# Kernel optimization log

Measured on AMD Instinct MI355X. Metric: run time of the kernel, lower is better.

The kernel has to match this reference:

```python
import jax, jax.numpy as jnp
import numpy as np

VD, VP, VM = 1958, 1430, 131
E = 64
B, S, ND, NM = 512, 16, 40, 30
SOS = VM  # voc_size[2]


def setup_inputs() -> dict:
    key = jax.random.key(0)
    ks = jax.random.split(key, 16)
    inp = {
        "diseases": jax.random.randint(ks[0], (B, S, ND), 0, VD),
        "procedures": jax.random.randint(ks[1], (B, S, 10), 0, VP),
        "medications": jax.random.randint(ks[2], (B, S, NM), 0, VM),
        "d_mask_matrix": jnp.zeros((B, S, ND), jnp.float32),
        "m_mask_matrix": jnp.zeros((B, S, NM), jnp.float32),
        "seq_length": jax.random.randint(ks[3], (B,), 1, S + 1),
    }
    s = 0.1
    inp["diag_table"] = s * jax.random.normal(ks[4], (VD + 3, E), jnp.float32)
    inp["med_table"] = s * jax.random.normal(ks[5], (VM + 3, E), jnp.float32)
    inp["attn_w"] = s * jax.random.normal(ks[6], (1, 2 * E), jnp.float32)
    inp["attn_b"] = jnp.zeros((1,), jnp.float32)
    inp["gru_w_ih"] = s * jax.random.normal(ks[7], (3 * E, 2 * E), jnp.float32)
    inp["gru_w_hh"] = s * jax.random.normal(ks[8], (3 * E, E), jnp.float32)
    inp["gru_b_ih"] = jnp.zeros((3 * E,), jnp.float32)
    inp["gru_b_hh"] = jnp.zeros((3 * E,), jnp.float32)
    inp["wo_w"] = s * jax.random.normal(ks[9], (VM + 2, E), jnp.float32)
    inp["wo_b"] = jnp.zeros((VM + 2,), jnp.float32)
    return inp


def reference(diseases, procedures, medications, d_mask_matrix, m_mask_matrix,
              seq_length, diag_table, med_table, attn_w, attn_b,
              gru_w_ih, gru_w_hh, gru_b_ih, gru_b_hh, wo_w, wo_b):
    # Training-mode (teacher-forcing) forward; dropout treated as identity (eval of dropout).
    b, s, nm = medications.shape
    e = diag_table.shape[1]
    disease_emb = diag_table[diseases]  # [B,S,Nd,E]
    # teacher-forcing inputs: SOS followed by gold medications
    last_med = jnp.concatenate(
        [jnp.full((b, s, 1), SOS, medications.dtype), medications], axis=2)  # [B,S,Nm+1]
    dec_embs = med_table[last_med]              # [B,S,Nm+1,E]
    xs = jnp.moveaxis(dec_embs, 2, 0)           # [T,B,S,E], T=Nm+1
    h0 = xs[0]                                  # hidden initialized to first dec input

    # additive attention: attn(concat([h, d])) = h @ w_h + d @ w_d + b
    w_h = attn_w[0, :e]
    w_d = attn_w[0, e:]
    d_score = jnp.einsum('bsne,e->bsn', disease_emb, w_d)  # precompute disease part

    def step(h, dec_input):
        score = d_score + jnp.einsum('bse,e->bs', h, w_h)[..., None] + attn_b[0]
        score = score + d_mask_matrix
        attn = jax.nn.softmax(score, axis=-1)               # [B,S,Nd]
        ctx = jnp.einsum('bsn,bsne->bse', attn, disease_emb)
        x = jnp.concatenate([ctx, dec_input], axis=-1)      # [B,S,2E]
        gi = x @ gru_w_ih.T + gru_b_ih
        gh = h @ gru_w_hh.T + gru_b_hh
        i_r, i_z, i_n = jnp.split(gi, 3, axis=-1)
        h_r, h_z, h_n = jnp.split(gh, 3, axis=-1)
        r = jax.nn.sigmoid(i_r + h_r)
        z = jax.nn.sigmoid(i_z + h_z)
        n = jnp.tanh(i_n + r * h_n)
        h_new = (1.0 - z) * n + z * h
        logit = jax.nn.log_softmax(h_new @ wo_w.T + wo_b, axis=-1)  # [B,S,Vm+2]
        return h_new, logit

    _, logits = jax.lax.scan(step, h0, xs)      # [T,B,S,Vm+2]
    return jnp.moveaxis(logits, 0, 2)           # [B,S,T,Vm+2]
```

## Files before the change

kernel.cpp:

```cpp
#include <hip/hip_runtime.h>
#include <math.h>

#define E_     64
#define ND_    40
#define NM_    30
#define NSTEP_ 31
#define VO_    133
#define J3_    192
#define NROW_  8192
#define RPB_   16
#define SOS_   131
#define NC_    344
#define NACT_  325

typedef __attribute__((ext_vector_type(8))) short short8;
typedef __attribute__((ext_vector_type(4))) float f32x4;

__device__ __forceinline__ float sigmoidf_(float x){ return 1.f/(1.f+__expf(-x)); }
__device__ __forceinline__ float tanhf_(float x){
  float ax = fabsf(x);
  float t = 1.f - 2.f/(__expf(2.f*ax)+1.f);
  return copysignf(t, x);
}
__device__ __forceinline__ unsigned short f2bf(float f){
  union { float f; unsigned u; } x; x.f = f;
  unsigned r = (x.u + 0x7fffu + ((x.u >> 16) & 1u)) >> 16;
  return (unsigned short)r;
}
__device__ __forceinline__ short8 pack8_(const float* __restrict__ s){
  short8 f;
  #pragma unroll
  for (int j=0;j<8;++j) f[j] = (short)f2bf(s[j]);
  return f;
}

__device__ __forceinline__ void bar_lds(){
  asm volatile("s_waitcnt lgkmcnt(0)" ::: "memory");
  __builtin_amdgcn_s_barrier();
  asm volatile("" ::: "memory");
}

__global__ __launch_bounds__(256) void k_pmed(const float* __restrict__ mt,
    const float* __restrict__ wih, float* __restrict__ pmed){
  int o = blockIdx.x*256 + threadIdx.x;
  if (o >= 134*J3_) return;
  int v = o / J3_, j = o - v*J3_;
  const float* mr = mt + v*E_;
  const float* wr = wih + j*128 + E_;
  float a = 0.f;
  #pragma unroll
  for (int k=0;k<E_;k++) a = fmaf(mr[k], wr[k], a);
  pmed[o] = a;
}

__global__ __launch_bounds__(512,4) void k_main(
    const int* __restrict__ dis, const float* __restrict__ dmask,
    const float* __restrict__ dt, const float* __restrict__ aw,
    const int* __restrict__ meds,
    const float* __restrict__ whh, const float* __restrict__ bhh,
    const float* __restrict__ wih, const float* __restrict__ bih,
    const float* __restrict__ wo, const float* __restrict__ wob,
    const float* __restrict__ mt, const float* __restrict__ pmed,
    float* __restrict__ out)
{
  __shared__ __align__(16) unsigned short hA[RPB_*E_];
  __shared__ __align__(16) float sC[RPB_*NC_];
  __shared__ int sLM[RPB_*32];

  const int tid = threadIdx.x;
  const int w = tid >> 6, l = tid & 63;
  const int l15 = l & 15, l4 = l >> 4;
  const int row = tid >> 5;
  const int d0  = (tid & 31) * 2;
  const int rowbase = blockIdx.x * RPB_;
  const int grow = rowbase + row;

  {
    int rr = tid >> 5, t = tid & 31;
    if (t < NSTEP_)
      sLM[rr*32 + t] = (t==0) ? SOS_ : meds[(size_t)(rowbase+rr)*NM_ + (t-1)];
  }

  float wd = aw[E_ + l];
  #pragma unroll 1
  for (int r2 = 0; r2 < 2; ++r2){
    int rr = 2*w + r2;
    const int*   drow = dis   + (size_t)(rowbase+rr)*ND_;
    const float* mrow = dmask + (size_t)(rowbase+rr)*ND_;
    float dreg[ND_], sc[ND_];
    float mx = -INFINITY;
    #pragma unroll
    for (int n = 0; n < ND_; ++n){
      float d = dt[(size_t)drow[n]*E_ + l];
      dreg[n] = d;
      float p = d * wd;
      #pragma unroll
      for (int m=1;m<64;m<<=1) p += __shfl_xor(p, m);
      sc[n] = p + mrow[n];
      mx = fmaxf(mx, sc[n]);
    }
    float ss = 0.f, ctx = 0.f;
    #pragma unroll
    for (int n = 0; n < ND_; ++n){
      float e = __expf(sc[n]-mx);
      ss += e;
      ctx = fmaf(e, dreg[n], ctx);
    }
    ctx /= ss;
    hA[rr*E_ + (l ^ ((rr&7)<<3))] = f2bf(ctx);
  }
  __syncthreads();

  {
    short8 A00 = *(const short8*)&hA[l15*E_ + ((l4*8     ) ^ ((l15&7)<<3))];
    short8 A01 = *(const short8*)&hA[l15*E_ + ((32 + l4*8) ^ ((l15&7)<<3))];
    #pragma unroll
    for (int jj = 0; jj < 2; ++jj){
      int n = w + 8*jj;
      if (n < 12){
        int c = n*16 + l15;
        short8 B0 = pack8_(wih + (size_t)c*128 + l4*8);
        short8 B1 = pack8_(wih + (size_t)c*128 + 32 + l4*8);
        f32x4 cc = {0.f,0.f,0.f,0.f};
        cc = __builtin_amdgcn_mfma_f32_16x16x32_bf16(A00, B0, cc, 0,0,0);
        cc = __builtin_amdgcn_mfma_f32_16x16x32_bf16(A01, B1, cc, 0,0,0);
        #pragma unroll
        for (int i=0;i<4;i++) sC[(l4*4+i)*NC_ + c] = cc[i];
      }
    }
  }
  __syncthreads();
  float2 gir = *(const float2*)&sC[row*NC_ + d0];
  float2 giz = *(const float2*)&sC[row*NC_ + d0 + 64];
  float2 gin = *(const float2*)&sC[row*NC_ + d0 + 128];
  {
    float2 a = *(const float2*)&bih[d0],      b = *(const float2*)&bhh[d0];
    float2 c = *(const float2*)&bih[d0+64],   d = *(const float2*)&bhh[d0+64];
    float2 e = *(const float2*)&bih[d0+128];
    gir.x += a.x + b.x; gir.y += a.y + b.y;
    giz.x += c.x + d.x; giz.y += c.y + d.y;
    gin.x += e.x;       gin.y += e.y;
  }
  float2 bhn = *(const float2*)&bhh[d0 + 128];
  float wbv[5];
  #pragma unroll
  for (int k = 0; k < 5; ++k){
    int idx = (tid&31) + 32*k;
    wbv[k] = (idx < VO_) ? wob[idx] : -1e30f;
  }

  short8 B0[3], B1[3];
  const int ntile = (w < 5) ? 3 : 2;
  #pragma unroll
  for (int j = 0; j < 3; ++j){
    short8 z = {0,0,0,0,0,0,0,0};
    B0[j] = z; B1[j] = z;
    if (j < ntile){
      int c = (w + 8*j)*16 + l15;
      #pragma unroll
      for (int ks = 0; ks < 2; ++ks){
        int k0 = ks*32 + l4*8;
        float v[8];
        if (c < J3_){
          const float* s = whh + (size_t)c*E_ + k0;
          #pragma unroll
          for (int jj=0;jj<8;jj++) v[jj] = s[jj];
        } else if (c < 192+VO_){
          const float* s = wo + (size_t)(c-192)*E_ + k0;
          #pragma unroll
          for (int jj=0;jj<8;jj++) v[jj] = s[jj];
        } else {
          #pragma unroll
          for (int jj=0;jj<8;jj++) v[jj] = 0.f;
        }
        short8 f;
        #pragma unroll
        for (int jj=0;jj<8;jj++) f[jj] = (short)f2bf(v[jj]);
        if (ks==0) B0[j] = f; else B1[j] = f;
      }
    }
  }

  float2 hv2 = *(const float2*)&mt[SOS_*E_ + d0];
  {
    unsigned hv = (unsigned)f2bf(hv2.x) | ((unsigned)f2bf(hv2.y)<<16);
    *(unsigned*)&hA[row*E_ + (d0 ^ ((row&7)<<3))] = hv;
  }
  __syncthreads();

  int lm = sLM[row*32];
  float2 pr = *(const float2*)&pmed[(size_t)lm*J3_ + d0];
  float2 pz = *(const float2*)&pmed[(size_t)lm*J3_ + d0 + 64];
  float2 pn = *(const float2*)&pmed[(size_t)lm*J3_ + d0 + 128];

  for (int t = 0; t <= NSTEP_; ++t){
    short8 A00 = *(const short8*)&hA[l15*E_ + ((l4*8     ) ^ ((l15&7)<<3))];
    short8 A01 = *(const short8*)&hA[l15*E_ + ((32 + l4*8) ^ ((l15&7)<<3))];
    #pragma unroll
    for (int j = 0; j < 3; ++j){
      if (j < ntile){
        f32x4 cc = {0.f,0.f,0.f,0.f};
        cc = __builtin_amdgcn_mfma_f32_16x16x32_bf16(A00, B0[j], cc, 0,0,0);
        cc = __builtin_amdgcn_mfma_f32_16x16x32_bf16(A01, B1[j], cc, 0,0,0);
        int c = (w + 8*j)*16 + l15;
        #pragma unroll
        for (int i=0;i<4;i++) sC[(l4*4+i)*NC_ + c] = cc[i];
      }
    }
    bar_lds();

    int lmn = 0; float2 npr, npz, npn;
    if (t+1 < NSTEP_){
      lmn = sLM[row*32 + t + 1];
      npr = *(const float2*)&pmed[(size_t)lmn*J3_ + d0];
      npz = *(const float2*)&pmed[(size_t)lmn*J3_ + d0 + 64];
      npn = *(const float2*)&pmed[(size_t)lmn*J3_ + d0 + 128];
    }

    if (t < NSTEP_){
      float2 ghr = *(const float2*)&sC[row*NC_ + d0];
      float2 ghz = *(const float2*)&sC[row*NC_ + d0 + 64];
      float2 ghn = *(const float2*)&sC[row*NC_ + d0 + 128];
      {
        float rg = sigmoidf_(gir.x + pr.x + ghr.x);
        float zg = sigmoidf_(giz.x + pz.x + ghz.x);
        float ng = tanhf_(gin.x + pn.x + rg*(ghn.x + bhn.x));
        hv2.x = (1.f - zg)*ng + zg*hv2.x;
      }
      {
        float rg = sigmoidf_(gir.y + pr.y + ghr.y);
        float zg = sigmoidf_(giz.y + pz.y + ghz.y);
        float ng = tanhf_(gin.y + pn.y + rg*(ghn.y + bhn.y));
        hv2.y = (1.f - zg)*ng + zg*hv2.y;
      }
      unsigned hv = (unsigned)f2bf(hv2.x) | ((unsigned)f2bf(hv2.y)<<16);
      *(unsigned*)&hA[row*E_ + (d0 ^ ((row&7)<<3))] = hv;
    }

    if (t >= 1){
      float lv[5]; float s = 0.f;
      #pragma unroll
      for (int k = 0; k < 5; ++k){
        int idx = (tid&31) + 32*k;
        lv[k] = (idx < VO_) ? (sC[row*NC_ + 192 + idx] + wbv[k]) : -1e30f;
        s += __expf(lv[k]);
      }
      #pragma unroll
      for (int mm=1; mm<32; mm<<=1) s += __shfl_xor(s, mm);
      float lg = __logf(s);
      size_t ob = ((size_t)grow*NSTEP_ + (t-1))*VO_;
      #pragma unroll
      for (int k = 0; k < 5; ++k){
        int idx = (tid&31) + 32*k;
        if (idx < VO_) out[ob + idx] = lv[k] - lg;
      }
    }
    bar_lds();

    if (t+1 < NSTEP_){ pr = npr; pz = npz; pn = npn; }
  }
}

extern "C" void kernel_launch(void* const* d_in, const int* in_sizes, int n_in,
                              void* d_out, int out_size, void* d_ws, size_t ws_size,
                              hipStream_t stream){
  const int*   dis  = (const int*)  d_in[0];
  const int*   meds = (const int*)  d_in[2];
  const float* dmask= (const float*)d_in[3];
  const float* dt   = (const float*)d_in[6];
  const float* mt   = (const float*)d_in[7];
  const float* aw   = (const float*)d_in[8];
  const float* wih  = (const float*)d_in[10];
  const float* whh  = (const float*)d_in[11];
  const float* bih  = (const float*)d_in[12];
  const float* bhh  = (const float*)d_in[13];
  const float* wo   = (const float*)d_in[14];
  const float* wob  = (const float*)d_in[15];
  float* outp = (float*)d_out;
  float* pmed = (float*)d_ws;

  k_pmed<<<(134*J3_+255)/256, 256, 0, stream>>>(mt, wih, pmed);
  k_main<<<NROW_/RPB_, 512, 0, stream>>>(dis, dmask, dt, aw, meds,
                                         whh, bhh, wih, bih, wo, wob,
                                         mt, pmed, outp);
}
```

Baseline: 97.92 us.

## Double-buffer MFMA output in LDS and defer log-softmax by one step

The gate/logit MFMA result buffer is split into two LDS buffers that alternate each timestep. The log-softmax and output store for the previous step now run in the same phase as the current step's MFMA, before the first barrier, so they no longer sit on the serial GRU critical path. The loop gains one extra iteration, and LDS usage roughly doubles for the result buffer, which may reduce how many blocks fit per CU. The logit indexing is also simplified with unrolled fixed offsets and a single predicate for the tail lanes.

```diff
diff --git a/kernel.cpp b/kernel.cpp
--- a/kernel.cpp
+++ b/kernel.cpp
@@ -10,8 +10,7 @@
 #define NROW_  8192
 #define RPB_   16
 #define SOS_   131
-#define NC_    344
-#define NACT_  325
+#define NC_    348
 
 typedef __attribute__((ext_vector_type(8))) short short8;
 typedef __attribute__((ext_vector_type(4))) float f32x4;
@@ -64,7 +63,8 @@
     float* __restrict__ out)
 {
   __shared__ __align__(16) unsigned short hA[RPB_*E_];
-  __shared__ __align__(16) float sC[RPB_*NC_];
+  __shared__ __align__(16) float sCa[RPB_*NC_];
+  __shared__ __align__(16) float sCb[RPB_*NC_];
   __shared__ int sLM[RPB_*32];
 
   const int tid = threadIdx.x;
@@ -72,6 +72,7 @@
   const int l15 = l & 15, l4 = l >> 4;
   const int row = tid >> 5;
   const int d0  = (tid & 31) * 2;
+  const int c32 = tid & 31;
   const int rowbase = blockIdx.x * RPB_;
   const int grow = rowbase + row;
 
@@ -125,14 +126,14 @@
         cc = __builtin_amdgcn_mfma_f32_16x16x32_bf16(A00, B0, cc, 0,0,0);
         cc = __builtin_amdgcn_mfma_f32_16x16x32_bf16(A01, B1, cc, 0,0,0);
         #pragma unroll
-        for (int i=0;i<4;i++) sC[(l4*4+i)*NC_ + c] = cc[i];
+        for (int i=0;i<4;i++) sCa[(l4*4+i)*NC_ + c] = cc[i];
       }
     }
   }
   __syncthreads();
-  float2 gir = *(const float2*)&sC[row*NC_ + d0];
-  float2 giz = *(const float2*)&sC[row*NC_ + d0 + 64];
-  float2 gin = *(const float2*)&sC[row*NC_ + d0 + 128];
+  float2 gir = *(const float2*)&sCa[row*NC_ + d0];
+  float2 giz = *(const float2*)&sCa[row*NC_ + d0 + 64];
+  float2 gin = *(const float2*)&sCa[row*NC_ + d0 + 128];
   {
     float2 a = *(const float2*)&bih[d0],      b = *(const float2*)&bhh[d0];
     float2 c = *(const float2*)&bih[d0+64],   d = *(const float2*)&bhh[d0+64];
@@ -144,10 +145,9 @@
   float2 bhn = *(const float2*)&bhh[d0 + 128];
   float wbv[5];
   #pragma unroll
-  for (int k = 0; k < 5; ++k){
-    int idx = (tid&31) + 32*k;
-    wbv[k] = (idx < VO_) ? wob[idx] : -1e30f;
-  }
+  for (int k = 0; k < 4; ++k) wbv[k] = wob[c32 + 32*k];
+  const bool v4 = (c32 < 5);
+  wbv[4] = v4 ? wob[c32 + 128] : 0.f;
 
   short8 B0[3], B1[3];
   const int ntile = (w < 5) ? 3 : 2;
@@ -193,34 +193,61 @@
   float2 pz = *(const float2*)&pmed[(size_t)lm*J3_ + d0 + 64];
   float2 pn = *(const float2*)&pmed[(size_t)lm*J3_ + d0 + 128];
 
-  for (int t = 0; t <= NSTEP_; ++t){
-    short8 A00 = *(const short8*)&hA[l15*E_ + ((l4*8     ) ^ ((l15&7)<<3))];
-    short8 A01 = *(const short8*)&hA[l15*E_ + ((32 + l4*8) ^ ((l15&7)<<3))];
-    #pragma unroll
-    for (int j = 0; j < 3; ++j){
-      if (j < ntile){
-        f32x4 cc = {0.f,0.f,0.f,0.f};
-        cc = __builtin_amdgcn_mfma_f32_16x16x32_bf16(A00, B0[j], cc, 0,0,0);
-        cc = __builtin_amdgcn_mfma_f32_16x16x32_bf16(A01, B1[j], cc, 0,0,0);
-        int c = (w + 8*j)*16 + l15;
-        #pragma unroll
-        for (int i=0;i<4;i++) sC[(l4*4+i)*NC_ + c] = cc[i];
-      }
-    }
-    bar_lds();
-
-    int lmn = 0; float2 npr, npz, npn;
+  float* opt = out + (size_t)grow*NSTEP_*VO_ + c32;
+
+  for (int t = 0; t <= NSTEP_+1; ++t){
+    float* cur  = (t & 1) ? sCb : sCa;
+    float* prev = (t & 1) ? sCa : sCb;
+
+    if (t <= NSTEP_){
+      short8 A00 = *(const short8*)&hA[l15*E_ + ((l4*8     ) ^ ((l15&7)<<3))];
+      short8 A01 = *(const short8*)&hA[l15*E_ + ((32 + l4*8) ^ ((l15&7)<<3))];
+      #pragma unroll
+      for (int j = 0; j < 3; ++j){
+        if (j < ntile){
+          f32x4 cc = {0.f,0.f,0.f,0.f};
+          cc = __builtin_amdgcn_mfma_f32_16x16x32_bf16(A00, B0[j], cc, 0,0,0);
+          cc = __builtin_amdgcn_mfma_f32_16x16x32_bf16(A01, B1[j], cc, 0,0,0);
+          int c = (w + 8*j)*16 + l15;
+          #pragma unroll
+          for (int i=0;i<4;i++) cur[(l4*4+i)*NC_ + c] = cc[i];
+        }
+      }
+    }
+
+    float2 npr={0.f,0.f}, npz={0.f,0.f}, npn={0.f,0.f};
     if (t+1 < NSTEP_){
-      lmn = sLM[row*32 + t + 1];
+      int lmn = sLM[row*32 + t + 1];
       npr = *(const float2*)&pmed[(size_t)lmn*J3_ + d0];
       npz = *(const float2*)&pmed[(size_t)lmn*J3_ + d0 + 64];
       npn = *(const float2*)&pmed[(size_t)lmn*J3_ + d0 + 128];
     }
 
+    if (t >= 2){
+      const float* pl = prev + row*NC_ + 192 + c32;
+      float lv0 = pl[0]   + wbv[0];
+      float lv1 = pl[32]  + wbv[1];
+      float lv2 = pl[64]  + wbv[2];
+      float lv3 = pl[96]  + wbv[3];
+      float lv4 = v4 ? (pl[128] + wbv[4]) : 0.f;
+      float s = __expf(lv0) + __expf(lv1) + __expf(lv2) + __expf(lv3)
+              + (v4 ? __expf(lv4) : 0.f);
+      #pragma unroll
+      for (int mm=1; mm<32; mm<<=1) s += __shfl_xor(s, mm);
+      float lg = __logf(s);
+      opt[0]  = lv0 - lg;
+      opt[32] = lv1 - lg;
+      opt[64] = lv2 - lg;
+      opt[96] = lv3 - lg;
+      if (v4) opt[128] = lv4 - lg;
+      opt += VO_;
+    }
+    bar_lds();
+
     if (t < NSTEP_){
-      float2 ghr = *(const float2*)&sC[row*NC_ + d0];
-      float2 ghz = *(const float2*)&sC[row*NC_ + d0 + 64];
-      float2 ghn = *(const float2*)&sC[row*NC_ + d0 + 128];
+      float2 ghr = *(const float2*)&cur[row*NC_ + d0];
+      float2 ghz = *(const float2*)&cur[row*NC_ + d0 + 64];
+      float2 ghn = *(const float2*)&cur[row*NC_ + d0 + 128];
       {
         float rg = sigmoidf_(gir.x + pr.x + ghr.x);
         float zg = sigmoidf_(giz.x + pz.x + ghz.x);
@@ -236,28 +263,9 @@
       unsigned hv = (unsigned)f2bf(hv2.x) | ((unsigned)f2bf(hv2.y)<<16);
       *(unsigned*)&hA[row*E_ + (d0 ^ ((row&7)<<3))] = hv;
     }
-
-    if (t >= 1){
-      float lv[5]; float s = 0.f;
-      #pragma unroll
-      for (int k = 0; k < 5; ++k){
-        int idx = (tid&31) + 32*k;
-        lv[k] = (idx < VO_) ? (sC[row*NC_ + 192 + idx] + wbv[k]) : -1e30f;
-        s += __expf(lv[k]);
-      }
-      #pragma unroll
-      for (int mm=1; mm<32; mm<<=1) s += __shfl_xor(s, mm);
-      float lg = __logf(s);
-      size_t ob = ((size_t)grow*NSTEP_ + (t-1))*VO_;
-      #pragma unroll
-      for (int k = 0; k < 5; ++k){
-        int idx = (tid&31) + 32*k;
-        if (idx < VO_) out[ob + idx] = lv[k] - lg;
-      }
-    }
     bar_lds();
 
-    if (t+1 < NSTEP_){ pr = npr; pz = npz; pn = npn; }
+    pr = npr; pz = npz; pn = npn;
   }
 }
 
```

New measurement: 101.4 us. 3.6% more time.

## Specialize warps into GRU and output-projection roles with double-buffered hidden state

Applied to the files above, without the earlier changes.

Splits the 8 waves of each block into 4 GRU waves that compute the recurrent matmul and gate math directly in MFMA registers, and 4 output waves that compute the vocabulary projection and log-softmax one step behind. The hidden state is double-buffered in LDS, so the output work for step t overlaps the recurrence for step t+1, and only one barrier per step is needed instead of two. This removes the shared sC round-trip for the gate results and the second barrier. In exchange the loop runs an extra pipeline step, the softmax sum takes a cross-wave LDS reduction, and load may be uneven between the two wave roles.

```diff
diff --git a/kernel.cpp b/kernel.cpp
--- a/kernel.cpp
+++ b/kernel.cpp
@@ -10,8 +10,7 @@
 #define NROW_  8192
 #define RPB_   16
 #define SOS_   131
-#define NC_    344
-#define NACT_  325
+#define NCP_   196
 
 typedef __attribute__((ext_vector_type(8))) short short8;
 typedef __attribute__((ext_vector_type(4))) float f32x4;
@@ -63,22 +62,23 @@
     const float* __restrict__ mt, const float* __restrict__ pmed,
     float* __restrict__ out)
 {
-  __shared__ __align__(16) unsigned short hA[RPB_*E_];
-  __shared__ __align__(16) float sC[RPB_*NC_];
+  __shared__ __align__(16) unsigned short hA[2][RPB_*E_];
+  __shared__ __align__(16) float sCp[RPB_*NCP_];
+  __shared__ __align__(16) float sPart[2][RPB_][4];
   __shared__ int sLM[RPB_*32];
 
   const int tid = threadIdx.x;
   const int w = tid >> 6, l = tid & 63;
   const int l15 = l & 15, l4 = l >> 4;
-  const int row = tid >> 5;
-  const int d0  = (tid & 31) * 2;
   const int rowbase = blockIdx.x * RPB_;
-  const int grow = rowbase + row;
+  const bool isg = (w < 4);
+  const int w4 = w - 4;
+  const int dcol = (w & 3)*16 + l15;
 
   {
-    int rr = tid >> 5, t = tid & 31;
-    if (t < NSTEP_)
-      sLM[rr*32 + t] = (t==0) ? SOS_ : meds[(size_t)(rowbase+rr)*NM_ + (t-1)];
+    int rr = tid >> 5, tt = tid & 31;
+    if (tt < NSTEP_)
+      sLM[rr*32 + tt] = (tt==0) ? SOS_ : meds[(size_t)(rowbase+rr)*NM_ + (tt-1)];
   }
 
   float wd = aw[E_ + l];
@@ -107,157 +107,186 @@
       ctx = fmaf(e, dreg[n], ctx);
     }
     ctx /= ss;
-    hA[rr*E_ + (l ^ ((rr&7)<<3))] = f2bf(ctx);
+    hA[0][rr*E_ + (l ^ ((rr&7)<<3))] = f2bf(ctx);
   }
   __syncthreads();
 
   {
-    short8 A00 = *(const short8*)&hA[l15*E_ + ((l4*8     ) ^ ((l15&7)<<3))];
-    short8 A01 = *(const short8*)&hA[l15*E_ + ((32 + l4*8) ^ ((l15&7)<<3))];
+    short8 A00 = *(const short8*)&hA[0][l15*E_ + (((l4  ) ^ (l15&7))<<3)];
+    short8 A01 = *(const short8*)&hA[0][l15*E_ + (((l4+4) ^ (l15&7))<<3)];
     #pragma unroll
     for (int jj = 0; jj < 2; ++jj){
       int n = w + 8*jj;
       if (n < 12){
         int c = n*16 + l15;
-        short8 B0 = pack8_(wih + (size_t)c*128 + l4*8);
-        short8 B1 = pack8_(wih + (size_t)c*128 + 32 + l4*8);
+        short8 Bp0 = pack8_(wih + (size_t)c*128 + l4*8);
+        short8 Bp1 = pack8_(wih + (size_t)c*128 + 32 + l4*8);
         f32x4 cc = {0.f,0.f,0.f,0.f};
-        cc = __builtin_amdgcn_mfma_f32_16x16x32_bf16(A00, B0, cc, 0,0,0);
-        cc = __builtin_amdgcn_mfma_f32_16x16x32_bf16(A01, B1, cc, 0,0,0);
+        cc = __builtin_amdgcn_mfma_f32_16x16x32_bf16(A00, Bp0, cc, 0,0,0);
+        cc = __builtin_amdgcn_mfma_f32_16x16x32_bf16(A01, Bp1, cc, 0,0,0);
         #pragma unroll
-        for (int i=0;i<4;i++) sC[(l4*4+i)*NC_ + c] = cc[i];
+        for (int i=0;i<4;i++) sCp[(l4*4+i)*NCP_ + c] = cc[i];
       }
     }
   }
   __syncthreads();
-  float2 gir = *(const float2*)&sC[row*NC_ + d0];
-  float2 giz = *(const float2*)&sC[row*NC_ + d0 + 64];
-  float2 gin = *(const float2*)&sC[row*NC_ + d0 + 128];
-  {
-    float2 a = *(const float2*)&bih[d0],      b = *(const float2*)&bhh[d0];
-    float2 c = *(const float2*)&bih[d0+64],   d = *(const float2*)&bhh[d0+64];
-    float2 e = *(const float2*)&bih[d0+128];
-    gir.x += a.x + b.x; gir.y += a.y + b.y;
-    giz.x += c.x + d.x; giz.y += c.y + d.y;
-    gin.x += e.x;       gin.y += e.y;
-  }
-  float2 bhn = *(const float2*)&bhh[d0 + 128];
-  float wbv[5];
-  #pragma unroll
-  for (int k = 0; k < 5; ++k){
-    int idx = (tid&31) + 32*k;
-    wbv[k] = (idx < VO_) ? wob[idx] : -1e30f;
-  }
-
-  short8 B0[3], B1[3];
-  const int ntile = (w < 5) ? 3 : 2;
-  #pragma unroll
-  for (int j = 0; j < 3; ++j){
+
+  short8 B0a, B1a, B0b, B1b, B0c, B1c;
+  float gia[4], giz[4], gin[4], hrv[4];
+  float pmr[4], pmz[4], pmn[4];
+  float bhn = 0.f;
+  float wbv0 = 0.f, wbv1 = 0.f, wbv2 = -1e30f;
+  float *pR0=0, *pR1=0, *pR2=0, *pR3=0;
+  const bool act2 = (w == 4);
+  const bool v2l  = (w == 4) && (l15 < 5);
+
+  if (isg){
+    float bi0 = bih[dcol] + bhh[dcol];
+    float bi1 = bih[dcol+64] + bhh[dcol+64];
+    float bi2 = bih[dcol+128];
+    bhn = bhh[dcol+128];
+    float h0 = mt[SOS_*E_ + dcol];
+    #pragma unroll
+    for (int i=0;i<4;++i){
+      int r = l4*4 + i;
+      gia[i] = sCp[r*NCP_ + dcol]       + bi0;
+      giz[i] = sCp[r*NCP_ + dcol + 64]  + bi1;
+      gin[i] = sCp[r*NCP_ + dcol + 128] + bi2;
+      hrv[i] = h0;
+      int lm = sLM[r*32];
+      const float* pp = pmed + (size_t)lm*J3_ + dcol;
+      pmr[i] = pp[0]; pmz[i] = pp[64]; pmn[i] = pp[128];
+      hA[0][r*E_ + ((((dcol>>3) ^ (r&7))<<3) + (dcol&7))] = f2bf(h0);
+    }
+    { int c = (w)*16 + l15;       B0a = pack8_(whh + (size_t)c*E_ + l4*8);
+                                  B1a = pack8_(whh + (size_t)c*E_ + 32 + l4*8); }
+    { int c = (w+4)*16 + l15;     B0b = pack8_(whh + (size_t)c*E_ + l4*8);
+                                  B1b = pack8_(whh + (size_t)c*E_ + 32 + l4*8); }
+    { int c = (w+8)*16 + l15;     B0c = pack8_(whh + (size_t)c*E_ + l4*8);
+                                  B1c = pack8_(whh + (size_t)c*E_ + 32 + l4*8); }
+  } else {
+    int c0 = w4*16 + l15;
+    int c1 = (w4+4)*16 + l15;
+    wbv0 = wob[c0];
+    wbv1 = wob[c1];
+    B0a = pack8_(wo + (size_t)c0*E_ + l4*8);
+    B1a = pack8_(wo + (size_t)c0*E_ + 32 + l4*8);
+    B0b = pack8_(wo + (size_t)c1*E_ + l4*8);
+    B1b = pack8_(wo + (size_t)c1*E_ + 32 + l4*8);
     short8 z = {0,0,0,0,0,0,0,0};
-    B0[j] = z; B1[j] = z;
-    if (j < ntile){
-      int c = (w + 8*j)*16 + l15;
-      #pragma unroll
-      for (int ks = 0; ks < 2; ++ks){
-        int k0 = ks*32 + l4*8;
-        float v[8];
-        if (c < J3_){
-          const float* s = whh + (size_t)c*E_ + k0;
+    B0c = z; B1c = z;
+    if (act2){
+      int c2 = 128 + l15;
+      if (c2 < VO_){
+        wbv2 = wob[c2];
+        B0c = pack8_(wo + (size_t)c2*E_ + l4*8);
+        B1c = pack8_(wo + (size_t)c2*E_ + 32 + l4*8);
+      }
+    }
+    pR0 = out + (size_t)(rowbase + l4*4 + 0)*NSTEP_*VO_;
+    pR1 = out + (size_t)(rowbase + l4*4 + 1)*NSTEP_*VO_;
+    pR2 = out + (size_t)(rowbase + l4*4 + 2)*NSTEP_*VO_;
+    pR3 = out + (size_t)(rowbase + l4*4 + 3)*NSTEP_*VO_;
+  }
+  f32x4 LP0 = {0.f,0.f,0.f,0.f}, LP1 = LP0, LP2 = LP0;
+  __syncthreads();
+
+  for (int t = 0; t <= NSTEP_+1; ++t){
+    const unsigned short* hc = hA[t&1];
+    if (isg){
+      if (t < NSTEP_){
+        short8 A00 = *(const short8*)&hc[l15*E_ + (((l4  ) ^ (l15&7))<<3)];
+        short8 A01 = *(const short8*)&hc[l15*E_ + (((l4+4) ^ (l15&7))<<3)];
+        f32x4 c0 = {0.f,0.f,0.f,0.f}, c1 = c0, c2 = c0;
+        c0 = __builtin_amdgcn_mfma_f32_16x16x32_bf16(A00, B0a, c0, 0,0,0);
+        c0 = __builtin_amdgcn_mfma_f32_16x16x32_bf16(A01, B1a, c0, 0,0,0);
+        c1 = __builtin_amdgcn_mfma_f32_16x16x32_bf16(A00, B0b, c1, 0,0,0);
+        c1 = __builtin_amdgcn_mfma_f32_16x16x32_bf16(A01, B1b, c1, 0,0,0);
+        c2 = __builtin_amdgcn_mfma_f32_16x16x32_bf16(A00, B0c, c2, 0,0,0);
+        c2 = __builtin_amdgcn_mfma_f32_16x16x32_bf16(A01, B1c, c2, 0,0,0);
+        unsigned short* hnw = hA[(t+1)&1];
+        #pragma unroll
+        for (int i=0;i<4;++i){
+          float ir = gia[i] + pmr[i] + c0[i];
+          float iz = giz[i] + pmz[i] + c1[i];
+          float nn = gin[i] + pmn[i];
+          float hn = c2[i] + bhn;
+          float rg = sigmoidf_(ir), zg = sigmoidf_(iz);
+          float ng = tanhf_(nn + rg*hn);
+          float h  = (1.f - zg)*ng + zg*hrv[i];
+          hrv[i] = h;
+          int r = l4*4 + i;
+          hnw[r*E_ + ((((dcol>>3) ^ (r&7))<<3) + (dcol&7))] = f2bf(h);
+        }
+        if (t+1 < NSTEP_){
           #pragma unroll
-          for (int jj=0;jj<8;jj++) v[jj] = s[jj];
-        } else if (c < 192+VO_){
-          const float* s = wo + (size_t)(c-192)*E_ + k0;
-          #pragma unroll
-          for (int jj=0;jj<8;jj++) v[jj] = s[jj];
-        } else {
-          #pragma unroll
-          for (int jj=0;jj<8;jj++) v[jj] = 0.f;
-        }
-        short8 f;
+          for (int i=0;i<4;++i){
+            int r = l4*4 + i;
+            int lm = sLM[r*32 + t + 1];
+            const float* pp = pmed + (size_t)lm*J3_ + dcol;
+            pmr[i] = pp[0]; pmz[i] = pp[64]; pmn[i] = pp[128];
+          }
+        }
+      }
+    } else {
+      f32x4 LC0 = {0.f,0.f,0.f,0.f}, LC1 = LC0, LC2 = LC0;
+      if (t >= 1 && t <= NSTEP_){
+        short8 A00 = *(const short8*)&hc[l15*E_ + (((l4  ) ^ (l15&7))<<3)];
+        short8 A01 = *(const short8*)&hc[l15*E_ + (((l4+4) ^ (l15&7))<<3)];
+        LC0 = __builtin_amdgcn_mfma_f32_16x16x32_bf16(A00, B0a, LC0, 0,0,0);
+        LC0 = __builtin_amdgcn_mfma_f32_16x16x32_bf16(A01, B1a, LC0, 0,0,0);
+        LC1 = __builtin_amdgcn_mfma_f32_16x16x32_bf16(A00, B0b, LC1, 0,0,0);
+        LC1 = __builtin_amdgcn_mfma_f32_16x16x32_bf16(A01, B1b, LC1, 0,0,0);
+        LC2 = __builtin_amdgcn_mfma_f32_16x16x32_bf16(A00, B0c, LC2, 0,0,0);
+        LC2 = __builtin_amdgcn_mfma_f32_16x16x32_bf16(A01, B1c, LC2, 0,0,0);
         #pragma unroll
-        for (int jj=0;jj<8;jj++) f[jj] = (short)f2bf(v[jj]);
-        if (ks==0) B0[j] = f; else B1[j] = f;
-      }
-    }
-  }
-
-  float2 hv2 = *(const float2*)&mt[SOS_*E_ + d0];
-  {
-    unsigned hv = (unsigned)f2bf(hv2.x) | ((unsigned)f2bf(hv2.y)<<16);
-    *(unsigned*)&hA[row*E_ + (d0 ^ ((row&7)<<3))] = hv;
-  }
-  __syncthreads();
-
-  int lm = sLM[row*32];
-  float2 pr = *(const float2*)&pmed[(size_t)lm*J3_ + d0];
-  float2 pz = *(const float2*)&pmed[(size_t)lm*J3_ + d0 + 64];
-  float2 pn = *(const float2*)&pmed[(size_t)lm*J3_ + d0 + 128];
-
-  for (int t = 0; t <= NSTEP_; ++t){
-    short8 A00 = *(const short8*)&hA[l15*E_ + ((l4*8     ) ^ ((l15&7)<<3))];
-    short8 A01 = *(const short8*)&hA[l15*E_ + ((32 + l4*8) ^ ((l15&7)<<3))];
-    #pragma unroll
-    for (int j = 0; j < 3; ++j){
-      if (j < ntile){
-        f32x4 cc = {0.f,0.f,0.f,0.f};
-        cc = __builtin_amdgcn_mfma_f32_16x16x32_bf16(A00, B0[j], cc, 0,0,0);
-        cc = __builtin_amdgcn_mfma_f32_16x16x32_bf16(A01, B1[j], cc, 0,0,0);
-        int c = (w + 8*j)*16 + l15;
+        for (int i=0;i<4;++i){
+          LC0[i] += wbv0; LC1[i] += wbv1; LC2[i] += wbv2;
+        }
+        float e0 = __expf(LC0[0]) + __expf(LC1[0]) + (act2 ? __expf(LC2[0]) : 0.f);
+        float e1 = __expf(LC0[1]) + __expf(LC1[1]) + (act2 ? __expf(LC2[1]) : 0.f);
+        float e2 = __expf(LC0[2]) + __expf(LC1[2]) + (act2 ? __expf(LC2[2]) : 0.f);
+        float e3 = __expf(LC0[3]) + __expf(LC1[3]) + (act2 ? __expf(LC2[3]) : 0.f);
         #pragma unroll
-        for (int i=0;i<4;i++) sC[(l4*4+i)*NC_ + c] = cc[i];
-      }
+        for (int mm=1; mm<16; mm<<=1){
+          e0 += __shfl_xor(e0, mm); e1 += __shfl_xor(e1, mm);
+          e2 += __shfl_xor(e2, mm); e3 += __shfl_xor(e3, mm);
+        }
+        if (l15 == 0){
+          int cb = t & 1;
+          sPart[cb][l4*4+0][w4] = e0;
+          sPart[cb][l4*4+1][w4] = e1;
+          sPart[cb][l4*4+2][w4] = e2;
+          sPart[cb][l4*4+3][w4] = e3;
+        }
+      }
+      if (t >= 2){
+        int pb = (t & 1) ^ 1;
+        f32x4 q0 = *(const f32x4*)&sPart[pb][l4*4+0][0];
+        f32x4 q1 = *(const f32x4*)&sPart[pb][l4*4+1][0];
+        f32x4 q2 = *(const f32x4*)&sPart[pb][l4*4+2][0];
+        f32x4 q3 = *(const f32x4*)&sPart[pb][l4*4+3][0];
+        float lg0 = __logf(q0[0]+q0[1]+q0[2]+q0[3]);
+        float lg1 = __logf(q1[0]+q1[1]+q1[2]+q1[3]);
+        float lg2 = __logf(q2[0]+q2[1]+q2[2]+q2[3]);
+        float lg3 = __logf(q3[0]+q3[1]+q3[2]+q3[3]);
+        int c0 = w4*16 + l15, c1 = (w4+4)*16 + l15;
+        pR0[c0] = LP0[0] - lg0;  pR0[c1] = LP1[0] - lg0;
+        pR1[c0] = LP0[1] - lg1;  pR1[c1] = LP1[1] - lg1;
+        pR2[c0] = LP0[2] - lg2;  pR2[c1] = LP1[2] - lg2;
+        pR3[c0] = LP0[3] - lg3;  pR3[c1] = LP1[3] - lg3;
+        if (v2l){
+          int c2 = 128 + l15;
+          pR0[c2] = LP2[0] - lg0;
+          pR1[c2] = LP2[1] - lg1;
+          pR2[c2] = LP2[2] - lg2;
+          pR3[c2] = LP2[3] - lg3;
+        }
+        pR0 += VO_; pR1 += VO_; pR2 += VO_; pR3 += VO_;
+      }
+      if (t >= 1 && t <= NSTEP_){ LP0 = LC0; LP1 = LC1; LP2 = LC2; }
     }
     bar_lds();
-
-    int lmn = 0; float2 npr, npz, npn;
-    if (t+1 < NSTEP_){
-      lmn = sLM[row*32 + t + 1];
-      npr = *(const float2*)&pmed[(size_t)lmn*J3_ + d0];
-      npz = *(const float2*)&pmed[(size_t)lmn*J3_ + d0 + 64];
-      npn = *(const float2*)&pmed[(size_t)lmn*J3_ + d0 + 128];
-    }
-
-    if (t < NSTEP_){
-      float2 ghr = *(const float2*)&sC[row*NC_ + d0];
-      float2 ghz = *(const float2*)&sC[row*NC_ + d0 + 64];
-      float2 ghn = *(const float2*)&sC[row*NC_ + d0 + 128];
-      {
-        float rg = sigmoidf_(gir.x + pr.x + ghr.x);
-        float zg = sigmoidf_(giz.x + pz.x + ghz.x);
-        float ng = tanhf_(gin.x + pn.x + rg*(ghn.x + bhn.x));
-        hv2.x = (1.f - zg)*ng + zg*hv2.x;
-      }
-      {
-        float rg = sigmoidf_(gir.y + pr.y + ghr.y);
-        float zg = sigmoidf_(giz.y + pz.y + ghz.y);
-        float ng = tanhf_(gin.y + pn.y + rg*(ghn.y + bhn.y));
-        hv2.y = (1.f - zg)*ng + zg*hv2.y;
-      }
-      unsigned hv = (unsigned)f2bf(hv2.x) | ((unsigned)f2bf(hv2.y)<<16);
-      *(unsigned*)&hA[row*E_ + (d0 ^ ((row&7)<<3))] = hv;
-    }
-
-    if (t >= 1){
-      float lv[5]; float s = 0.f;
-      #pragma unroll
-      for (int k = 0; k < 5; ++k){
-        int idx = (tid&31) + 32*k;
-        lv[k] = (idx < VO_) ? (sC[row*NC_ + 192 + idx] + wbv[k]) : -1e30f;
-        s += __expf(lv[k]);
-      }
-      #pragma unroll
-      for (int mm=1; mm<32; mm<<=1) s += __shfl_xor(s, mm);
-      float lg = __logf(s);
-      size_t ob = ((size_t)grow*NSTEP_ + (t-1))*VO_;
-      #pragma unroll
-      for (int k = 0; k < 5; ++k){
-        int idx = (tid&31) + 32*k;
-        if (idx < VO_) out[ob + idx] = lv[k] - lg;
-      }
-    }
-    bar_lds();
-
-    if (t+1 < NSTEP_){ pr = npr; pz = npz; pn = npn; }
   }
 }
 
```

Measured after the change: 108.6 us. 1.11x slower.
